# Kernel tuning notes

Hardware: AMD Instinct MI355X
Metric: run time of the kernel (lower is better)

## Reference

```python
import jax, jax.numpy as jnp
import numpy as np

B, S, D, H = 4, 1024, 1024, 16
DK = D // H


def setup_inputs() -> dict:
    key = jax.random.key(0)
    ks = jax.random.split(key, 14)
    scale = 1.0 / np.sqrt(D)
    inp = {
        "Qx": jax.random.normal(ks[0], (B, S, D), jnp.float32),
        "Kx": jax.random.normal(ks[1], (B, S, D), jnp.float32),
        "Vx": jax.random.normal(ks[2], (B, S, D), jnp.float32),
        "prob_phn": jax.random.uniform(ks[3], (B, S, S), jnp.float32),
        "mask": jax.random.randint(ks[4], (B, S, S), 0, 2, jnp.int32),
        "lambda_val": 1,
        "Wq": jax.random.normal(ks[5], (D, D), jnp.float32) * scale,
        "bq": jnp.zeros((D,), jnp.float32),
        "Wk": jax.random.normal(ks[6], (D, D), jnp.float32) * scale,
        "bk": jnp.zeros((D,), jnp.float32),
        "Wv": jax.random.normal(ks[7], (D, D), jnp.float32) * scale,
        "bv": jnp.zeros((D,), jnp.float32),
        "Wo": jax.random.normal(ks[8], (D, D), jnp.float32) * scale,
        "bo": jnp.zeros((D,), jnp.float32),
    }
    return inp


def _split_heads(x):
    # [B,S,D] -> [B,H,S,DK]
    b, s, _ = x.shape
    return x.reshape(b, s, H, DK).transpose(0, 2, 1, 3)


def reference(Qx, Kx, Vx, prob_phn, mask, lambda_val, Wq, bq, Wk, bk, Wv, bv, Wo, bo):
    q = _split_heads(Qx @ Wq.T + bq)
    k = _split_heads(Kx @ Wk.T + bk)
    v = _split_heads(Vx @ Wv.T + bv)
    scores = jnp.einsum("bhqd,bhkd->bhqk", q, k) / jnp.sqrt(jnp.float32(DK))
    if lambda_val > 0:
        # prob_phn: [B,S,S] -> transpose last two dims, broadcast over heads
        scores = scores - lambda_val * jnp.swapaxes(prob_phn, -2, -1)[:, None]
    scores = jnp.where(mask[:, None] == 0, jnp.float32(-1e9), scores)
    probs = jax.nn.softmax(scores, axis=-1)
    attn = jnp.einsum("bhqk,bhkd->bhqd", probs, v)
    out = attn.transpose(0, 2, 1, 3).reshape(Qx.shape[0], Qx.shape[1], D)
    out = out @ Wo.T + bo
    return (out, mask)
```

## Files before the change

kernel.cpp:

```cpp
#include <hip/hip_runtime.h>
#include <hip/hip_bf16.h>
#include <cstdint>
#include <cstddef>

#define BB 4
#define SS 1024
#define DD 1024
#define HH 16
#define DKK 64

typedef unsigned short u16;
typedef __bf16 bf16_t;
typedef __attribute__((ext_vector_type(8))) bf16_t bf16x8;
typedef __attribute__((ext_vector_type(4))) float floatx4;

#define LOG2E 1.4426950408889634f
#define QKSCALE 0.18033688011112042f

static __device__ inline u16 f2bf(float f) {
    union { float f; unsigned u; } v; v.f = f;
    unsigned r = v.u + 0x7fffu + ((v.u >> 16) & 1u);
    return (u16)(r >> 16);
}

static __device__ inline void load16_lds(const void* g, void* l) {
    __builtin_amdgcn_global_load_lds(
        (const __attribute__((address_space(1))) unsigned int*)g,
        (__attribute__((address_space(3))) unsigned int*)l,
        16, 0, 0);
}

static __device__ inline int swz64(int row, int c) { return row * 64 + ((c ^ (row & 7)) * 8); }

static __device__ inline float lam_val(const int* p) {
    int v = *p;
    if (v >= -100000 && v <= 100000) return (float)v;
    union { int i; float f; } u; u.i = v; return u.f;
}

__global__ void prep_kernel(const float* __restrict__ Qx, const float* __restrict__ Kx,
                            const float* __restrict__ Vx,
                            const float* __restrict__ Wq, const float* __restrict__ Wk,
                            const float* __restrict__ Wv, const float* __restrict__ Wo,
                            const float* __restrict__ prob, const int* __restrict__ mask,
                            const int* __restrict__ lam_p,
                            u16* __restrict__ Xq, u16* __restrict__ Xk, u16* __restrict__ Xv,
                            u16* __restrict__ wq, u16* __restrict__ wk,
                            u16* __restrict__ wv, u16* __restrict__ wo,
                            u16* __restrict__ biasT, float* __restrict__ maskOut)
{
    __shared__ union {
        float tile[64][65];
        u16   btile[64][68];
    } sh;
    const int blk = blockIdx.x, tid = threadIdx.x;

    if (blk >= 1024) {
        const int cb = blk - 1024;
        const int base = cb * 1024;
        const float* src; u16* dst; int off0;
        if (base < 3145728) {
            int s = base >> 20;  off0 = base & 1048575;
            src = (s == 0) ? Qx : (s == 1) ? Kx : Vx;
            dst = (s == 0) ? Xq : (s == 1) ? Xk : Xv;
        } else {
            int v2 = base - 3145728;
            int s = v2 >> 18;  off0 = v2 & 262143;
            src = (s == 0) ? Wq : (s == 1) ? Wk : (s == 2) ? Wv : Wo;
            dst = (s == 0) ? wq : (s == 1) ? wk : (s == 2) ? wv : wo;
        }
        const float4* s4 = (const float4*)src;
        #pragma unroll
        for (int r = 0; r < 2; ++r) {
            int i4 = off0 + r * 512 + tid * 2;
            float4 a  = s4[i4];
            float4 b2 = s4[i4 + 1];
            uint4 pk;
            pk.x = (unsigned)f2bf(a.x)  | ((unsigned)f2bf(a.y)  << 16);
            pk.y = (unsigned)f2bf(a.z)  | ((unsigned)f2bf(a.w)  << 16);
            pk.z = (unsigned)f2bf(b2.x) | ((unsigned)f2bf(b2.y) << 16);
            pk.w = (unsigned)f2bf(b2.z) | ((unsigned)f2bf(b2.w) << 16);
            *(uint4*)((ushort4*)dst + i4) = pk;
        }
        return;
    }

    const int b = blk >> 8;
    const int q0 = ((blk >> 4) & 15) * 64, k0 = (blk & 15) * 64;
    const int kt = blk & 15;
    #pragma unroll
    for (int rr = 0; rr < 4; ++rr) {
        int unit = rr * 256 + tid;
        int kl = unit >> 4, qi = unit & 15;
        float4 p4 = *(const float4*)&prob[((size_t)(b * SS + k0 + kl)) * SS + q0 + qi * 4];
        sh.tile[kl][qi * 4 + 0] = p4.x;
        sh.tile[kl][qi * 4 + 1] = p4.y;
        sh.tile[kl][qi * 4 + 2] = p4.z;
        sh.tile[kl][qi * 4 + 3] = p4.w;
    }
    __syncthreads();
    const float lamc = lam_val(lam_p) * LOG2E;
    ushort4 bbv[4];
    int qv[4], k4v[4];
    #pragma unroll
    for (int rr = 0; rr < 4; ++rr) {
        int pair = rr * 256 + tid;
        int q = pair >> 4, k4 = pair & 15;
        qv[rr] = q; k4v[rr] = k4;
        size_t midx = ((size_t)(b * SS + q0 + q)) * SS + k0 + k4 * 4;
        int4 m4 = *(const int4*)&mask[midx];
        float p0 = sh.tile[k4 * 4 + 0][q];
        float p1 = sh.tile[k4 * 4 + 1][q];
        float p2 = sh.tile[k4 * 4 + 2][q];
        float p3 = sh.tile[k4 * 4 + 3][q];
        bbv[rr].x = f2bf((m4.x == 0) ? -1.5e9f : -lamc * p0);
        bbv[rr].y = f2bf((m4.y == 0) ? -1.5e9f : -lamc * p1);
        bbv[rr].z = f2bf((m4.z == 0) ? -1.5e9f : -lamc * p2);
        bbv[rr].w = f2bf((m4.w == 0) ? -1.5e9f : -lamc * p3);
        if (maskOut) {
            float4 mf = { (float)m4.x, (float)m4.y, (float)m4.z, (float)m4.w };
            *(float4*)&maskOut[midx] = mf;
        }
    }
    __syncthreads();
    #pragma unroll
    for (int rr = 0; rr < 4; ++rr)
        *(ushort4*)&sh.btile[qv[rr]][k4v[rr] * 4] = bbv[rr];
    __syncthreads();
    u16* bT = biasT + (size_t)(b * 16 + kt) * 65536;
    #pragma unroll
    for (int rr = 0; rr < 4; ++rr) {
        int idx = rr * 256 + tid;
        int j = idx >> 8, quad = (idx >> 6) & 3, ql = idx & 63;
        ushort4 v = *(const ushort4*)&sh.btile[ql][j * 16 + quad * 4];
        *(ushort4*)&bT[(size_t)((j * 4 + quad) * 1024 + q0 + ql) * 4] = v;
    }
}

template <int MODE>
static __device__ inline void gemm_body(const u16* __restrict__ A, const u16* __restrict__ W,
                                        const float* __restrict__ bias,
                                        u16* __restrict__ Cb, float* __restrict__ Cf,
                                        int mBase, int nBase,
                                        u16* As, u16* Bs)
{
    constexpr int K = 1024, N = 1024;
    const int tid = threadIdx.x;
    const int wv = tid >> 6, ln = tid & 63, l15 = ln & 15, quad = ln >> 4;
    const int wm = (wv & 1) * 64, wn = (wv >> 1) * 64;

    const u16* Aptr[4]; const u16* Wptr[4];
    #pragma unroll
    for (int r = 0; r < 4; ++r) {
        int p = r * 256 + wv * 64 + ln;
        int row = p >> 3;
        int c = (p & 7) ^ (row & 7);
        Aptr[r] = A + (size_t)(mBase + row) * K + c * 8;
        Wptr[r] = W + (size_t)(nBase + row) * K + c * 8;
    }

    floatx4 acc[4][4] = {};

    for (int k0 = 0; k0 < K; k0 += 64) {
        __syncthreads();
        #pragma unroll
        for (int r = 0; r < 4; ++r) {
            load16_lds(Aptr[r] + k0, &As[(r * 256 + wv * 64) * 8]);
            load16_lds(Wptr[r] + k0, &Bs[(r * 256 + wv * 64) * 8]);
        }
        __syncthreads();
        #pragma unroll
        for (int t = 0; t < 2; ++t) {
            bf16x8 af[4], bfr[4];
            #pragma unroll
            for (int i = 0; i < 4; ++i)
                af[i] = *(const bf16x8*)&As[swz64(wm + i * 16 + l15, t * 4 + quad)];
            #pragma unroll
            for (int j = 0; j < 4; ++j)
                bfr[j] = *(const bf16x8*)&Bs[swz64(wn + j * 16 + l15, t * 4 + quad)];
            #pragma unroll
            for (int i = 0; i < 4; ++i)
                #pragma unroll
                for (int j = 0; j < 4; ++j)
                    acc[i][j] = __builtin_amdgcn_mfma_f32_16x16x32_bf16(af[i], bfr[j], acc[i][j], 0, 0, 0);
        }
    }

    #pragma unroll
    for (int i = 0; i < 4; ++i) {
        #pragma unroll
        for (int j = 0; j < 4; ++j) {
            int col = nBase + wn + j * 16 + l15;
            float bcol = bias[col];
            if (MODE == 2) {
                int hh = col >> 6, dk = col & 63;
                int row0 = mBase + wm + i * 16 + quad * 4;
                int bb = row0 >> 10, s = row0 & 1023;
                ushort4 v4;
                v4.x = f2bf(acc[i][j][0] + bcol);
                v4.y = f2bf(acc[i][j][1] + bcol);
                v4.z = f2bf(acc[i][j][2] + bcol);
                v4.w = f2bf(acc[i][j][3] + bcol);
                *(ushort4*)&Cb[((size_t)((bb * HH + hh) * DKK) + dk) * SS + s] = v4;
            } else {
                #pragma unroll
                for (int r = 0; r < 4; ++r) {
                    int row = mBase + wm + i * 16 + quad * 4 + r;
                    float v = acc[i][j][r] + bcol;
                    if (MODE == 1) Cf[(size_t)row * N + col] = v;
                    else           Cb[(size_t)row * N + col] = f2bf(v);
                }
            }
        }
    }
}

__global__ __launch_bounds__(256) void gemm_qkv_kernel(
    const u16* __restrict__ Xq, const u16* __restrict__ Xk, const u16* __restrict__ Xv,
    const u16* __restrict__ Wq, const u16* __restrict__ Wk, const u16* __restrict__ Wv,
    const float* __restrict__ bq, const float* __restrict__ bk, const float* __restrict__ bv,
    u16* __restrict__ Cq, u16* __restrict__ Ck, u16* __restrict__ Vtout)
{
    __shared__ __align__(16) u16 As[128 * 64];
    __shared__ __align__(16) u16 Bs[128 * 64];

    const int lin = blockIdx.x + 8 * blockIdx.y + 256 * blockIdx.z;
    const int sw  = (lin & 7) * 96 + (lin >> 3);
    const int x = sw & 7, y = (sw >> 3) & 31, z = sw >> 8;
    const int mBase = y * 128, nBase = x * 128;

    if (z == 2) {
        gemm_body<2>(Xv, Wv, bv, Vtout, nullptr, mBase, nBase, As, Bs);
    } else {
        const u16* A = (z == 0) ? Xq : Xk;
        const u16* W = (z == 0) ? Wq : Wk;
        const float* bias = (z == 0) ? bq : bk;
        u16* C = (z == 0) ? Cq : Ck;
        gemm_body<0>(A, W, bias, C, nullptr, mBase, nBase, As, Bs);
    }
}

__global__ __launch_bounds__(256) void gemm_out_kernel(
    const u16* __restrict__ A, const u16* __restrict__ W,
    const float* __restrict__ bias, float* __restrict__ Cf)
{
    __shared__ __align__(16) u16 As[128 * 64];
    __shared__ __align__(16) u16 Bs[128 * 64];

    const int lin = blockIdx.x + 8 * blockIdx.y;
    const int sw  = (lin & 7) * 32 + (lin >> 3);
    const int x = sw & 7, y = sw >> 3;
    gemm_body<1>(A, W, bias, nullptr, Cf, y * 128, x * 128, As, Bs);
}

__global__ __launch_bounds__(256) void attn_kernel(
    const u16* __restrict__ Qf, const u16* __restrict__ Kf,
    const u16* __restrict__ Vt, const u16* __restrict__ biasT,
    u16* __restrict__ Attn)
{
    __shared__ __align__(16) u16 Qs[64 * 64];
    __shared__ __align__(16) u16 Ks[64 * 64];
    __shared__ __align__(16) u16 Vs[64 * 64];
    __shared__ __align__(16) u16 Ps[4][16 * 72];
    const int tid = threadIdx.x;
    const int wv = tid >> 6, ln = tid & 63, l15 = ln & 15, quad = ln >> 4;

    const int lin = blockIdx.x + 16 * blockIdx.y + 256 * blockIdx.z;
    const int sw  = (lin & 7) * 128 + (lin >> 3);
    const int qt = sw & 15, h = (sw >> 4) & 15, b = sw >> 8;
    const int q0 = qt * 64;

    int row64[2], col64[2];
    #pragma unroll
    for (int r = 0; r < 2; ++r) {
        int p = r * 256 + wv * 64 + ln;
        row64[r] = p >> 3;
        col64[r] = ((p & 7) ^ (row64[r] & 7)) * 8;
    }

    #pragma unroll
    for (int r = 0; r < 2; ++r)
        load16_lds(Qf + ((size_t)(b * SS + q0 + row64[r])) * DD + h * DKK + col64[r],
                   &Qs[(r * 256 + wv * 64) * 8]);
    __syncthreads();

    bf16x8 aq[2];
    #pragma unroll
    for (int t = 0; t < 2; ++t)
        aq[t] = *(const bf16x8*)&Qs[swz64(wv * 16 + l15, t * 4 + quad)];

    const size_t vt_head = ((size_t)(b * HH + h)) * DKK * SS;
    const u16* Kp[2]; const u16* Vp[2];
    #pragma unroll
    for (int r = 0; r < 2; ++r) {
        Kp[r] = Kf + ((size_t)(b * SS + row64[r])) * DD + h * DKK + col64[r];
        Vp[r] = Vt + vt_head + (size_t)row64[r] * SS + col64[r];
    }

    const int qq = q0 + wv * 16 + l15;
    const u16* bpT = biasT + (size_t)b * 1048576 + (size_t)quad * 4096 + (size_t)qq * 4;

    floatx4 o[4] = {};
    float rsum = 0.f;

    for (int kt = 0; kt < 16; ++kt) {
        const int kk0 = kt * 64;
        __syncthreads();
        #pragma unroll
        for (int r = 0; r < 2; ++r) {
            load16_lds(Kp[r] + (size_t)kk0 * DD, &Ks[(r * 256 + wv * 64) * 8]);
            load16_lds(Vp[r] + kk0, &Vs[(r * 256 + wv * 64) * 8]);
        }
        __syncthreads();

        uint2 braw[4];
        #pragma unroll
        for (int j = 0; j < 4; ++j)
            braw[j] = *(const uint2*)&bpT[(size_t)kt * 65536 + j * 16384];

        floatx4 sfr[4];
        #pragma unroll
        for (int j = 0; j < 4; ++j) {
            bf16x8 bk0 = *(const bf16x8*)&Ks[swz64(j * 16 + l15, quad)];
            bf16x8 bk1 = *(const bf16x8*)&Ks[swz64(j * 16 + l15, 4 + quad)];
            floatx4 s = {};
            s = __builtin_amdgcn_mfma_f32_16x16x32_bf16(bk0, aq[0], s, 0, 0, 0);
            sfr[j] = __builtin_amdgcn_mfma_f32_16x16x32_bf16(bk1, aq[1], s, 0, 0, 0);
        }

        #pragma unroll
        for (int j = 0; j < 4; ++j) {
            float b0 = __uint_as_float(braw[j].x << 16);
            float b1 = __uint_as_float(braw[j].x & 0xffff0000u);
            float b2 = __uint_as_float(braw[j].y << 16);
            float b3 = __uint_as_float(braw[j].y & 0xffff0000u);
            float p0 = __builtin_amdgcn_exp2f(fmaf(sfr[j][0], QKSCALE, b0));
            float p1 = __builtin_amdgcn_exp2f(fmaf(sfr[j][1], QKSCALE, b1));
            float p2 = __builtin_amdgcn_exp2f(fmaf(sfr[j][2], QKSCALE, b2));
            float p3 = __builtin_amdgcn_exp2f(fmaf(sfr[j][3], QKSCALE, b3));
            rsum += (p0 + p1) + (p2 + p3);
            uint2 pk;
            pk.x = (__float_as_uint(p0) >> 16) | (__float_as_uint(p1) & 0xffff0000u);
            pk.y = (__float_as_uint(p2) >> 16) | (__float_as_uint(p3) & 0xffff0000u);
            *(uint2*)&Ps[wv][l15 * 72 + j * 16 + quad * 4] = pk;
        }

        #pragma unroll
        for (int t = 0; t < 2; ++t) {
            bf16x8 ap = *(const bf16x8*)&Ps[wv][l15 * 72 + t * 32 + quad * 8];
            #pragma unroll
            for (int j = 0; j < 4; ++j) {
                bf16x8 bvv = *(const bf16x8*)&Vs[swz64(j * 16 + l15, t * 4 + quad)];
                o[j] = __builtin_amdgcn_mfma_f32_16x16x32_bf16(bvv, ap, o[j], 0, 0, 0);
            }
        }
    }

    rsum += __shfl_xor(rsum, 16);
    rsum += __shfl_xor(rsum, 32);
    const float ri = 1.0f / rsum;

    u16* outp = Attn + ((size_t)(b * SS + qq)) * DD + h * DKK + quad * 4;
    #pragma unroll
    for (int j = 0; j < 4; ++j) {
        ushort4 v4;
        v4.x = f2bf(o[j][0] * ri);
        v4.y = f2bf(o[j][1] * ri);
        v4.z = f2bf(o[j][2] * ri);
        v4.w = f2bf(o[j][3] * ri);
        *(ushort4*)&outp[j * 16] = v4;
    }
}

extern "C" void kernel_launch(void* const* d_in, const int* in_sizes, int n_in,
                              void* d_out, int out_size, void* d_ws, size_t ws_size,
                              hipStream_t stream)
{
    const float* Qx  = (const float*)d_in[0];
    const float* Kx  = (const float*)d_in[1];
    const float* Vx  = (const float*)d_in[2];
    const float* prob = (const float*)d_in[3];
    const int*   mask = (const int*)d_in[4];
    const int*   lam  = (const int*)d_in[5];
    const float* Wq  = (const float*)d_in[6];
    const float* bq  = (const float*)d_in[7];
    const float* Wk  = (const float*)d_in[8];
    const float* bk  = (const float*)d_in[9];
    const float* Wv  = (const float*)d_in[10];
    const float* bv  = (const float*)d_in[11];
    const float* Wo  = (const float*)d_in[12];
    const float* bo  = (const float*)d_in[13];

    char* ws = (char*)d_ws;
    const size_t MB = 1024 * 1024;
    u16*   Xq     = (u16*)(ws + 0 * MB);
    u16*   Xk     = (u16*)(ws + 8 * MB);
    u16*   Xv     = (u16*)(ws + 16 * MB);
    u16*   wq     = (u16*)(ws + 24 * MB);
    u16*   wk     = (u16*)(ws + 26 * MB);
    u16*   wvp    = (u16*)(ws + 28 * MB);
    u16*   wo     = (u16*)(ws + 30 * MB);
    u16*   q_flat = (u16*)(ws + 32 * MB);
    u16*   k_flat = (u16*)(ws + 40 * MB);
    u16*   vt     = (u16*)(ws + 56 * MB);
    u16*   biasT  = (u16*)(ws + 64 * MB);
    u16*   attn   = (u16*)(ws + 80 * MB);

    float* maskOut = (out_size >= 2 * BB * SS * DD) ? (float*)d_out + (size_t)BB * SS * DD
                                                    : nullptr;

    prep_kernel<<<5120, 256, 0, stream>>>(Qx, Kx, Vx, Wq, Wk, Wv, Wo, prob, mask, lam,
                                          Xq, Xk, Xv, wq, wk, wvp, wo, biasT, maskOut);
    gemm_qkv_kernel<<<dim3(8, 32, 3), 256, 0, stream>>>(Xq, Xk, Xv, wq, wk, wvp,
                                                        bq, bk, bv, q_flat, k_flat, vt);
    attn_kernel<<<dim3(16, 16, 4), 256, 0, stream>>>(q_flat, k_flat, vt, biasT, attn);
    gemm_out_kernel<<<dim3(8, 32, 1), 256, 0, stream>>>(attn, wo, bo, (float*)d_out);
}
```

Measured before the change: 248.5 us.

## Double-buffer QKV GEMM with BK=32 stages and split output GEMM into 64-row tiles

```diff
diff --git a/kernel.cpp b/kernel.cpp
--- a/kernel.cpp
+++ b/kernel.cpp
@@ -31,6 +31,7 @@
 }
 
 static __device__ inline int swz64(int row, int c) { return row * 64 + ((c ^ (row & 7)) * 8); }
+static __device__ inline int swz32(int row, int c) { return row * 32 + ((c ^ ((row >> 1) & 3)) * 8); }
 
 static __device__ inline float lam_val(const int* p) {
     int v = *p;
@@ -138,53 +139,67 @@
 }
 
 template <int MODE>
-static __device__ inline void gemm_body(const u16* __restrict__ A, const u16* __restrict__ W,
-                                        const float* __restrict__ bias,
-                                        u16* __restrict__ Cb, float* __restrict__ Cf,
-                                        int mBase, int nBase,
-                                        u16* As, u16* Bs)
+static __device__ inline void gemm_body32(const u16* __restrict__ A, const u16* __restrict__ W,
+                                          const float* __restrict__ bias,
+                                          u16* __restrict__ Cb, float* __restrict__ Cf,
+                                          int mBase, int nBase,
+                                          u16* As0, u16* Bs0, u16* As1, u16* Bs1)
 {
     constexpr int K = 1024, N = 1024;
     const int tid = threadIdx.x;
     const int wv = tid >> 6, ln = tid & 63, l15 = ln & 15, quad = ln >> 4;
     const int wm = (wv & 1) * 64, wn = (wv >> 1) * 64;
 
-    const u16* Aptr[4]; const u16* Wptr[4];
-    #pragma unroll
-    for (int r = 0; r < 4; ++r) {
+    const u16* Aptr[2]; const u16* Wptr[2];
+    #pragma unroll
+    for (int r = 0; r < 2; ++r) {
         int p = r * 256 + wv * 64 + ln;
-        int row = p >> 3;
-        int c = (p & 7) ^ (row & 7);
+        int row = p >> 2;
+        int c = (p & 3) ^ ((row >> 1) & 3);
         Aptr[r] = A + (size_t)(mBase + row) * K + c * 8;
         Wptr[r] = W + (size_t)(nBase + row) * K + c * 8;
     }
 
     floatx4 acc[4][4] = {};
 
+#define G_STAGE32(k0, Ad, Bd)                                            \
+    {                                                                    \
+        _Pragma("unroll")                                                \
+        for (int r = 0; r < 2; ++r) {                                    \
+            load16_lds(Aptr[r] + (k0), &Ad[(r * 256 + wv * 64) * 8]);    \
+            load16_lds(Wptr[r] + (k0), &Bd[(r * 256 + wv * 64) * 8]);    \
+        }                                                                \
+    }
+
+#define G_COMPUTE32(Asrc, Bsrc)                                          \
+    {                                                                    \
+        bf16x8 af[4], bfr[4];                                            \
+        _Pragma("unroll")                                                \
+        for (int i = 0; i < 4; ++i)                                      \
+            af[i] = *(const bf16x8*)&Asrc[swz32(wm + i * 16 + l15, quad)]; \
+        _Pragma("unroll")                                                \
+        for (int j = 0; j < 4; ++j)                                      \
+            bfr[j] = *(const bf16x8*)&Bsrc[swz32(wn + j * 16 + l15, quad)]; \
+        _Pragma("unroll")                                                \
+        for (int i = 0; i < 4; ++i)                                      \
+            _Pragma("unroll")                                            \
+            for (int j = 0; j < 4; ++j)                                  \
+                acc[i][j] = __builtin_amdgcn_mfma_f32_16x16x32_bf16(af[i], bfr[j], acc[i][j], 0, 0, 0); \
+    }
+
+    G_STAGE32(0, As0, Bs0);
+    __syncthreads();
+
     for (int k0 = 0; k0 < K; k0 += 64) {
-        __syncthreads();
-        #pragma unroll
-        for (int r = 0; r < 4; ++r) {
-            load16_lds(Aptr[r] + k0, &As[(r * 256 + wv * 64) * 8]);
-            load16_lds(Wptr[r] + k0, &Bs[(r * 256 + wv * 64) * 8]);
-        }
-        __syncthreads();
-        #pragma unroll
-        for (int t = 0; t < 2; ++t) {
-            bf16x8 af[4], bfr[4];
-            #pragma unroll
-            for (int i = 0; i < 4; ++i)
-                af[i] = *(const bf16x8*)&As[swz64(wm + i * 16 + l15, t * 4 + quad)];
-            #pragma unroll
-            for (int j = 0; j < 4; ++j)
-                bfr[j] = *(const bf16x8*)&Bs[swz64(wn + j * 16 + l15, t * 4 + quad)];
-            #pragma unroll
-            for (int i = 0; i < 4; ++i)
-                #pragma unroll
-                for (int j = 0; j < 4; ++j)
-                    acc[i][j] = __builtin_amdgcn_mfma_f32_16x16x32_bf16(af[i], bfr[j], acc[i][j], 0, 0, 0);
-        }
-    }
+        if (k0 + 32 < K) G_STAGE32(k0 + 32, As1, Bs1);
+        G_COMPUTE32(As0, Bs0);
+        __syncthreads();
+        if (k0 + 64 < K) G_STAGE32(k0 + 64, As0, Bs0);
+        G_COMPUTE32(As1, Bs1);
+        __syncthreads();
+    }
+#undef G_STAGE32
+#undef G_COMPUTE32
 
     #pragma unroll
     for (int i = 0; i < 4; ++i) {
@@ -207,22 +222,24 @@
                 for (int r = 0; r < 4; ++r) {
                     int row = mBase + wm + i * 16 + quad * 4 + r;
                     float v = acc[i][j][r] + bcol;
-                    if (MODE == 1) Cf[(size_t)row * N + col] = v;
-                    else           Cb[(size_t)row * N + col] = f2bf(v);
+                    (void)Cf;
+                    Cb[(size_t)row * N + col] = f2bf(v);
                 }
             }
         }
     }
 }
 
-__global__ __launch_bounds__(256) void gemm_qkv_kernel(
+__global__ __launch_bounds__(256, 3) void gemm_qkv_kernel(
     const u16* __restrict__ Xq, const u16* __restrict__ Xk, const u16* __restrict__ Xv,
     const u16* __restrict__ Wq, const u16* __restrict__ Wk, const u16* __restrict__ Wv,
     const float* __restrict__ bq, const float* __restrict__ bk, const float* __restrict__ bv,
     u16* __restrict__ Cq, u16* __restrict__ Ck, u16* __restrict__ Vtout)
 {
-    __shared__ __align__(16) u16 As[128 * 64];
-    __shared__ __align__(16) u16 Bs[128 * 64];
+    __shared__ __align__(16) u16 As0[128 * 32];
+    __shared__ __align__(16) u16 Bs0[128 * 32];
+    __shared__ __align__(16) u16 As1[128 * 32];
+    __shared__ __align__(16) u16 Bs1[128 * 32];
 
     const int lin = blockIdx.x + 8 * blockIdx.y + 256 * blockIdx.z;
     const int sw  = (lin & 7) * 96 + (lin >> 3);
@@ -230,13 +247,13 @@
     const int mBase = y * 128, nBase = x * 128;
 
     if (z == 2) {
-        gemm_body<2>(Xv, Wv, bv, Vtout, nullptr, mBase, nBase, As, Bs);
+        gemm_body32<2>(Xv, Wv, bv, Vtout, nullptr, mBase, nBase, As0, Bs0, As1, Bs1);
     } else {
         const u16* A = (z == 0) ? Xq : Xk;
         const u16* W = (z == 0) ? Wq : Wk;
         const float* bias = (z == 0) ? bq : bk;
         u16* C = (z == 0) ? Cq : Ck;
-        gemm_body<0>(A, W, bias, C, nullptr, mBase, nBase, As, Bs);
+        gemm_body32<0>(A, W, bias, C, nullptr, mBase, nBase, As0, Bs0, As1, Bs1);
     }
 }
 
@@ -244,13 +261,75 @@
     const u16* __restrict__ A, const u16* __restrict__ W,
     const float* __restrict__ bias, float* __restrict__ Cf)
 {
-    __shared__ __align__(16) u16 As[128 * 64];
+    constexpr int K = 1024, N = 1024;
+    __shared__ __align__(16) u16 As[64 * 64];
     __shared__ __align__(16) u16 Bs[128 * 64];
+    const int tid = threadIdx.x;
+    const int wv = tid >> 6, ln = tid & 63, l15 = ln & 15, quad = ln >> 4;
+    const int wn = wv * 32;
 
     const int lin = blockIdx.x + 8 * blockIdx.y;
-    const int sw  = (lin & 7) * 32 + (lin >> 3);
+    const int sw  = (lin & 7) * 64 + (lin >> 3);
     const int x = sw & 7, y = sw >> 3;
-    gemm_body<1>(A, W, bias, nullptr, Cf, y * 128, x * 128, As, Bs);
+    const int mBase = y * 64, nBase = x * 128;
+
+    const u16* Aptr[2]; const u16* Wptr[4];
+    #pragma unroll
+    for (int r = 0; r < 2; ++r) {
+        int p = r * 256 + wv * 64 + ln;
+        int row = p >> 3;
+        int c = (p & 7) ^ (row & 7);
+        Aptr[r] = A + (size_t)(mBase + row) * K + c * 8;
+    }
+    #pragma unroll
+    for (int r = 0; r < 4; ++r) {
+        int p = r * 256 + wv * 64 + ln;
+        int row = p >> 3;
+        int c = (p & 7) ^ (row & 7);
+        Wptr[r] = W + (size_t)(nBase + row) * K + c * 8;
+    }
+
+    floatx4 acc[4][2] = {};
+
+    for (int k0 = 0; k0 < K; k0 += 64) {
+        __syncthreads();
+        #pragma unroll
+        for (int r = 0; r < 2; ++r)
+            load16_lds(Aptr[r] + k0, &As[(r * 256 + wv * 64) * 8]);
+        #pragma unroll
+        for (int r = 0; r < 4; ++r)
+            load16_lds(Wptr[r] + k0, &Bs[(r * 256 + wv * 64) * 8]);
+        __syncthreads();
+        #pragma unroll
+        for (int t = 0; t < 2; ++t) {
+            bf16x8 af[4], bfr[2];
+            #pragma unroll
+            for (int i = 0; i < 4; ++i)
+                af[i] = *(const bf16x8*)&As[swz64(i * 16 + l15, t * 4 + quad)];
+            #pragma unroll
+            for (int j = 0; j < 2; ++j)
+                bfr[j] = *(const bf16x8*)&Bs[swz64(wn + j * 16 + l15, t * 4 + quad)];
+            #pragma unroll
+            for (int i = 0; i < 4; ++i)
+                #pragma unroll
+                for (int j = 0; j < 2; ++j)
+                    acc[i][j] = __builtin_amdgcn_mfma_f32_16x16x32_bf16(af[i], bfr[j], acc[i][j], 0, 0, 0);
+        }
+    }
+
+    #pragma unroll
+    for (int i = 0; i < 4; ++i) {
+        #pragma unroll
+        for (int j = 0; j < 2; ++j) {
+            int col = nBase + wn + j * 16 + l15;
+            float bcol = bias[col];
+            #pragma unroll
+            for (int r = 0; r < 4; ++r) {
+                int row = mBase + i * 16 + quad * 4 + r;
+                Cf[(size_t)row * N + col] = acc[i][j][r] + bcol;
+            }
+        }
+    }
 }
 
 __global__ __launch_bounds__(256) void attn_kernel(
@@ -414,5 +493,5 @@
     gemm_qkv_kernel<<<dim3(8, 32, 3), 256, 0, stream>>>(Xq, Xk, Xv, wq, wk, wvp,
                                                         bq, bk, bv, q_flat, k_flat, vt);
     attn_kernel<<<dim3(16, 16, 4), 256, 0, stream>>>(q_flat, k_flat, vt, biasT, attn);
-    gemm_out_kernel<<<dim3(8, 32, 1), 256, 0, stream>>>(attn, wo, bo, (float*)d_out);
-}
+    gemm_out_kernel<<<dim3(8, 64), 256, 0, stream>>>(attn, wo, bo, (float*)d_out);
+}
```

After: 242.4 us. 1.03x faster.
